# Kernel optimization log

Hardware: AMD Instinct MI355X
Metric: run time of the kernel (lower is better)

## Reference

```python
import jax, jax.numpy as jnp
import numpy as np

N = 100000          # nodes
E = 6400000         # edges (avg degree 64)
D = 512             # in_dim
NEG_SLOPE = 0.2     # PyG GATConv default leaky_relu slope


def setup_inputs() -> dict:
    key = jax.random.key(0)
    k1, k2, k3, k4, k5 = jax.random.split(key, 5)
    F = jax.random.normal(k1, (N, D), dtype=jnp.float32)
    edge_index = jax.random.randint(k2, (2, E), 0, N)
    W = jax.random.normal(k3, (D, 1), dtype=jnp.float32) * 0.05   # lin weight, out_channels=1
    att_src = jax.random.normal(k4, (1,), dtype=jnp.float32) * 0.1
    att_dst = jax.random.normal(k5, (1,), dtype=jnp.float32) * 0.1
    bias = jnp.zeros((1,), dtype=jnp.float32)
    return {"F": F, "edge_index": edge_index, "W": W,
            "att_src": att_src, "att_dst": att_dst, "bias": bias}


def reference(F, edge_index, W, att_src, att_dst, bias):
    n = F.shape[0]
    x = F @ W                                   # [N, 1] projected features
    # PyG GATConv default: add self-loops
    loops = jnp.arange(n, dtype=edge_index.dtype)
    src = jnp.concatenate([edge_index[0], loops])   # message source j
    dst = jnp.concatenate([edge_index[1], loops])   # message destination i
    a_src = (x * att_src).sum(-1)               # [N]
    a_dst = (x * att_dst).sum(-1)               # [N]
    logits = jax.nn.leaky_relu(a_src[src] + a_dst[dst], NEG_SLOPE)  # [E+N]
    # numerically stable per-destination softmax over incoming edges
    m = jax.ops.segment_max(logits, dst, num_segments=n)
    e = jnp.exp(logits - m[dst])
    denom = jax.ops.segment_sum(e, dst, num_segments=n)
    alpha = e / denom[dst]                      # [E+N]
    out = jax.ops.segment_sum(alpha[:, None] * x[src], dst, num_segments=n)  # [N,1]
    out = out + bias
    return out.squeeze()                        # [N]
```

## Files before the change

### kernel.cpp

```cpp
#include <hip/hip_runtime.h>

#define NEG_SLOPE 0.2f

#define DEN_SCALE 524288.0f
#define NUM_SCALE 32768.0f
#define INV_DEN_SCALE (1.0f / 524288.0f)
#define INV_NUM_SCALE (1.0f / 32768.0f)

#define RBITS 12
#define RSZ   4096
#define MAXNB 64
#define SSUB  16
#define EPT   8
#define P1BLK 256
#define CHUNK (P1BLK * EPT)

typedef float v4f __attribute__((ext_vector_type(4)));
typedef int   v4i __attribute__((ext_vector_type(4)));
typedef unsigned long long u64;
typedef unsigned int u32;

__global__ void gemv_rowdot(const float* __restrict__ F, const float* __restrict__ W,
                            float* __restrict__ x, int n, int d) {
    int wave = (blockIdx.x * blockDim.x + threadIdx.x) >> 6;
    int lane = threadIdx.x & 63;
    if (wave >= n) return;
    const v4f* f4 = (const v4f*)(F + (size_t)wave * d);
    const v4f* w4 = (const v4f*)W;
    int nv = d >> 2;
    float s = 0.f;
    #pragma unroll 2
    for (int k = lane; k < nv; k += 64) {
        v4f a = __builtin_nontemporal_load(&f4[k]);
        v4f b = w4[k];
        s += a.x * b.x + a.y * b.y + a.z * b.z + a.w * b.w;
    }
    #pragma unroll
    for (int off = 32; off; off >>= 1) s += __shfl_down(s, off, 64);
    if (lane == 0) x[wave] = s;
}

__device__ __forceinline__ u64 pack_edge(float e, float xs, int dlow) {
    int den = __float2int_rn(e * DEN_SCALE);
    den = min(den, (1 << 26) - 1);
    int num = __float2int_rn(e * xs * NUM_SCALE);
    num = max(min(num, (1 << 25) - 1), -((1 << 25) - 1));
    return (u64)(u32)dlow | ((u64)(u32)den << RBITS) | ((u64)((u32)num & 0x3FFFFFFu) << 38);
}

__global__ __launch_bounds__(P1BLK)
void bucket_scatter(const int* __restrict__ ei, const float* __restrict__ x,
                    const float* __restrict__ att_src_p, const float* __restrict__ att_dst_p,
                    u64* __restrict__ binbuf, u32* __restrict__ cnt,
                    u64* __restrict__ acc, int nedges, int nb, int capb) {
    __shared__ u32 lhist[MAXNB];
    __shared__ u32 lbase[MAXNB];
    const int tid = threadIdx.x;
    for (int b = tid; b < nb; b += P1BLK) lhist[b] = 0;
    __syncthreads();

    const long long base_e = (long long)blockIdx.x * CHUNK + (long long)tid * EPT;
    const float as = *att_src_p, ad = *att_dst_p;

    int se[EPT], de[EPT];
    if (((nedges & 3) == 0) && (base_e + EPT <= nedges)) {
        const v4i* sp = (const v4i*)(ei + base_e);
        const v4i* dp = (const v4i*)(ei + (size_t)nedges + base_e);
        v4i a0 = sp[0], a1 = sp[1], b0 = dp[0], b1 = dp[1];
        se[0] = a0.x; se[1] = a0.y; se[2] = a0.z; se[3] = a0.w;
        se[4] = a1.x; se[5] = a1.y; se[6] = a1.z; se[7] = a1.w;
        de[0] = b0.x; de[1] = b0.y; de[2] = b0.z; de[3] = b0.w;
        de[4] = b1.x; de[5] = b1.y; de[6] = b1.z; de[7] = b1.w;
    } else {
        #pragma unroll
        for (int t = 0; t < EPT; ++t) {
            long long idx = base_e + t;
            if (idx < nedges) { se[t] = ei[idx]; de[t] = ei[(size_t)nedges + idx]; }
            else { se[t] = -1; de[t] = -1; }
        }
    }

    float xs[EPT], xd[EPT];
    #pragma unroll
    for (int t = 0; t < EPT; ++t)
        if (se[t] >= 0) { xs[t] = x[se[t]]; xd[t] = x[de[t]]; }

    u64 pk[EPT]; u32 rk[EPT]; int bn[EPT];
    #pragma unroll
    for (int t = 0; t < EPT; ++t) {
        if (se[t] >= 0) {
            float v = xs[t] * as + xd[t] * ad;
            float logit = v > 0.f ? v : NEG_SLOPE * v;
            float e = __expf(logit);
            bn[t] = de[t] >> RBITS;
            pk[t] = pack_edge(e, xs[t], de[t] & (RSZ - 1));
            rk[t] = atomicAdd(&lhist[bn[t]], 1u);
        } else {
            bn[t] = -1;
        }
    }
    __syncthreads();
    if (tid < nb) lbase[tid] = atomicAdd(&cnt[tid], lhist[tid]);
    __syncthreads();
    #pragma unroll
    for (int t = 0; t < EPT; ++t) {
        if (bn[t] >= 0) {
            u32 slot = lbase[bn[t]] + rk[t];
            if (slot < (u32)capb) {
                binbuf[(size_t)bn[t] * (size_t)capb + slot] = pk[t];
            } else {
                int num = (int)((long long)pk[t] >> 38);
                u32 den = (u32)((pk[t] >> RBITS) & 0x3FFFFFFu);
                int dd = (bn[t] << RBITS) | (int)(pk[t] & (u64)(RSZ - 1));
                atomicAdd(&acc[dd], ((u64)(u32)num << 32) | (u64)den);
            }
        }
    }
}

__global__ __launch_bounds__(1024)
void bin_reduce(const u64* __restrict__ binbuf, const u32* __restrict__ cnt,
                u64* __restrict__ partial, int nb, int capb) {
    __shared__ u64 lacc[RSZ];
    const int b = blockIdx.x / SSUB;
    const int s = blockIdx.x % SSUB;
    const int tid = threadIdx.x;
    #pragma unroll
    for (int r = tid; r < RSZ; r += 1024) lacc[r] = 0ull;
    __syncthreads();

    u32 cb = cnt[b];
    if (cb > (u32)capb) cb = (u32)capb;
    u32 lo = (u32)(((u64)cb * (u32)s) / SSUB);
    u32 hi = (u32)(((u64)cb * (u32)(s + 1)) / SSUB);
    const u64* src = binbuf + (size_t)b * (size_t)capb;
    for (u32 k = lo + tid; k < hi; k += 1024) {
        u64 p = src[k];
        u32 r   = (u32)(p & (u64)(RSZ - 1));
        u32 den = (u32)((p >> RBITS) & 0x3FFFFFFu);
        int num = (int)((long long)p >> 38);
        atomicAdd(&lacc[r], ((u64)(u32)num << 32) | (u64)den);
    }
    __syncthreads();
    u64* dstp = partial + (size_t)blockIdx.x * RSZ;
    #pragma unroll
    for (int r = tid; r < RSZ; r += 1024) dstp[r] = lacc[r];
}

__global__ void finalize2(const u64* __restrict__ partial, const u64* __restrict__ acc,
                          const float* __restrict__ x,
                          const float* __restrict__ att_src_p,
                          const float* __restrict__ att_dst_p,
                          const float* __restrict__ bias, float* __restrict__ out, int n) {
    int i = blockIdx.x * blockDim.x + threadIdx.x;
    if (i >= n) return;
    int b = i >> RBITS, r = i & (RSZ - 1);
    u64 t = acc[i];
    const u64* pp = partial + ((size_t)b * SSUB) * RSZ + r;
    #pragma unroll
    for (int s = 0; s < SSUB; ++s) t += pp[(size_t)s * RSZ];
    float xi = x[i];
    float v = xi * (*att_src_p + *att_dst_p);
    float logit = v > 0.f ? v : NEG_SLOPE * v;
    float es = __expf(logit);
    float num = (float)(int)(t >> 32) * INV_NUM_SCALE;
    float den = (float)(u32)(t & 0xFFFFFFFFull) * INV_DEN_SCALE;
    out[i] = (num + es * xi) / (den + es) + *bias;
}

__device__ __forceinline__ void edge_one(float xs, float xd, float as, float ad,
                                         int d, u64* __restrict__ acc) {
    float v = xs * as + xd * ad;
    float logit = v > 0.f ? v : NEG_SLOPE * v;
    float e = __expf(logit);
    u32 den_fx = (u32)__float2int_rn(e * DEN_SCALE);
    int num_fx = __float2int_rn(e * xs * NUM_SCALE);
    atomicAdd(&acc[d], ((u64)(u32)num_fx << 32) | (u64)den_fx);
}

__global__ void edge_accum4(const int* __restrict__ ei, const float* __restrict__ x,
                            const float* __restrict__ att_src_p,
                            const float* __restrict__ att_dst_p,
                            u64* __restrict__ acc, int nedges) {
    int nq = nedges >> 2;
    int i = blockIdx.x * blockDim.x + threadIdx.x;
    if (i >= nq) return;
    const v4i* s4 = (const v4i*)ei;
    const v4i* d4 = (const v4i*)(ei + nedges);
    v4i s = s4[i], d = d4[i];
    float as = *att_src_p, ad = *att_dst_p;
    float xs0 = x[s.x], xs1 = x[s.y], xs2 = x[s.z], xs3 = x[s.w];
    float xd0 = x[d.x], xd1 = x[d.y], xd2 = x[d.z], xd3 = x[d.w];
    edge_one(xs0, xd0, as, ad, d.x, acc);
    edge_one(xs1, xd1, as, ad, d.y, acc);
    edge_one(xs2, xd2, as, ad, d.z, acc);
    edge_one(xs3, xd3, as, ad, d.w, acc);
}

__global__ void edge_accum1(const int* __restrict__ ei, const float* __restrict__ x,
                            const float* __restrict__ att_src_p,
                            const float* __restrict__ att_dst_p,
                            u64* __restrict__ acc, int nedges) {
    int i = blockIdx.x * blockDim.x + threadIdx.x;
    if (i >= nedges) return;
    int s = ei[i], d = ei[nedges + i];
    edge_one(x[s], x[d], *att_src_p, *att_dst_p, d, acc);
}

__global__ void finalize_atomic(const u64* __restrict__ acc, const float* __restrict__ x,
                                const float* __restrict__ att_src_p,
                                const float* __restrict__ att_dst_p,
                                const float* __restrict__ bias, float* __restrict__ out,
                                int n) {
    int i = blockIdx.x * blockDim.x + threadIdx.x;
    if (i >= n) return;
    float xi = x[i];
    float v = xi * (*att_src_p + *att_dst_p);
    float logit = v > 0.f ? v : NEG_SLOPE * v;
    float es = __expf(logit);
    u64 a = acc[i];
    float num = (float)(int)(a >> 32) * INV_NUM_SCALE;
    float den = (float)(u32)(a & 0xFFFFFFFFull) * INV_DEN_SCALE;
    out[i] = (num + es * xi) / (den + es) + *bias;
}

extern "C" void kernel_launch(void* const* d_in, const int* in_sizes, int n_in,
                              void* d_out, int out_size, void* d_ws, size_t ws_size,
                              hipStream_t stream) {
    const float* F       = (const float*)d_in[0];
    const int*   ei      = (const int*)d_in[1];
    const float* W       = (const float*)d_in[2];
    const float* att_src = (const float*)d_in[3];
    const float* att_dst = (const float*)d_in[4];
    const float* bias    = (const float*)d_in[5];
    float* out = (float*)d_out;

    int d = in_sizes[2];
    int n = in_sizes[0] / d;
    int e = in_sizes[1] / 2;

    int nb = (n + RSZ - 1) >> RBITS;
    size_t capb_s = ((size_t)e * RSZ) / (size_t)n;
    capb_s += capb_s / 16 + 4096;
    int capb = (int)capb_s;

    size_t off_x   = 0;
    size_t off_acc = ((size_t)n * 4 + 7) & ~(size_t)7;
    size_t off_cnt = off_acc + (size_t)n * 8;
    size_t off_par = (off_cnt + (size_t)nb * 4 + 7) & ~(size_t)7;
    size_t off_bin = off_par + (size_t)nb * SSUB * RSZ * 8;
    size_t needed  = off_bin + (size_t)nb * capb_s * 8;

    float* x  = (float*)((char*)d_ws + off_x);
    u64* acc  = (u64*)((char*)d_ws + off_acc);
    u32* cnt  = (u32*)((char*)d_ws + off_cnt);
    u64* par  = (u64*)((char*)d_ws + off_par);
    u64* bin  = (u64*)((char*)d_ws + off_bin);

    bool fast = (nb <= MAXNB) && (needed <= ws_size) && (e > 0) && (n > 0);

    gemv_rowdot<<<(n + 3) / 4, 256, 0, stream>>>(F, W, x, n, d);

    if (fast) {
        (void)hipMemsetAsync(acc, 0, (size_t)n * 8 + (size_t)nb * 4, stream);
        int nblk1 = (int)(((long long)e + CHUNK - 1) / CHUNK);
        bucket_scatter<<<nblk1, P1BLK, 0, stream>>>(ei, x, att_src, att_dst,
                                                    bin, cnt, acc, e, nb, capb);
        bin_reduce<<<nb * SSUB, 1024, 0, stream>>>(bin, cnt, par, nb, capb);
        finalize2<<<(n + 255) / 256, 256, 0, stream>>>(par, acc, x, att_src, att_dst,
                                                       bias, out, n);
    } else {
        (void)hipMemsetAsync(acc, 0, (size_t)n * 8, stream);
        if (e > 0) {
            if ((e & 3) == 0) {
                edge_accum4<<<((e >> 2) + 255) / 256, 256, 0, stream>>>(
                    ei, x, att_src, att_dst, acc, e);
            } else {
                edge_accum1<<<(e + 255) / 256, 256, 0, stream>>>(
                    ei, x, att_src, att_dst, acc, e);
            }
        }
        finalize_atomic<<<(n + 255) / 256, 256, 0, stream>>>(acc, x, att_src, att_dst,
                                                             bias, out, n);
    }
}
```

Measured before the change: 377.5 us.

## Fuse GEMV with edge bucketing and defer logit computation to bin reduce

The bucket scatter no longer depends on x. It packs (src, dst-low) into 32-bit bin entries, and its blocks run in the same launch as the GEMV blocks, so the edge-index bucketing overlaps with the large F read. Logit, exp and fixed-point packing move to bin_reduce, which keeps the bucket's destination x values in shared memory and gathers x[src] from global. Bin entries are half as wide, overflow edges go to a separate buffer handled by a new kernel, and EPT/SSUB are raised. The cost is an extra launch and random x[src] gathers in the reduce phase.

```diff
diff --git a/kernel.cpp b/kernel.cpp
--- a/kernel.cpp
+++ b/kernel.cpp
@@ -10,15 +10,26 @@
 #define RBITS 12
 #define RSZ   4096
 #define MAXNB 64
-#define SSUB  16
-#define EPT   8
+#define SSUB  20
+#define EPT   16
 #define P1BLK 256
 #define CHUNK (P1BLK * EPT)
+#define P2BLK 1024
 
 typedef float v4f __attribute__((ext_vector_type(4)));
 typedef int   v4i __attribute__((ext_vector_type(4)));
 typedef unsigned long long u64;
 typedef unsigned int u32;
+
+__device__ __forceinline__ void edge_one(float xs, float xd, float as, float ad,
+                                         int d, u64* __restrict__ acc) {
+    float v = xs * as + xd * ad;
+    float logit = v > 0.f ? v : NEG_SLOPE * v;
+    float e = __expf(logit);
+    u32 den_fx = (u32)__float2int_rn(e * DEN_SCALE);
+    int num_fx = __float2int_rn(e * xs * NUM_SCALE);
+    atomicAdd(&acc[d], ((u64)(u32)num_fx << 32) | (u64)den_fx);
+}
 
 __global__ void gemv_rowdot(const float* __restrict__ F, const float* __restrict__ W,
                             float* __restrict__ x, int n, int d) {
@@ -40,19 +51,32 @@
     if (lane == 0) x[wave] = s;
 }
 
-__device__ __forceinline__ u64 pack_edge(float e, float xs, int dlow) {
-    int den = __float2int_rn(e * DEN_SCALE);
-    den = min(den, (1 << 26) - 1);
-    int num = __float2int_rn(e * xs * NUM_SCALE);
-    num = max(min(num, (1 << 25) - 1), -((1 << 25) - 1));
-    return (u64)(u32)dlow | ((u64)(u32)den << RBITS) | ((u64)((u32)num & 0x3FFFFFFu) << 38);
-}
-
 __global__ __launch_bounds__(P1BLK)
-void bucket_scatter(const int* __restrict__ ei, const float* __restrict__ x,
-                    const float* __restrict__ att_src_p, const float* __restrict__ att_dst_p,
-                    u64* __restrict__ binbuf, u32* __restrict__ cnt,
-                    u64* __restrict__ acc, int nedges, int nb, int capb) {
+void gemv_and_scatter(const float* __restrict__ F, const float* __restrict__ W,
+                      float* __restrict__ x, int n, int d,
+                      const int* __restrict__ ei, u32* __restrict__ binbuf,
+                      u32* __restrict__ cnt, u64* __restrict__ ovf,
+                      int nedges, int nb, int capb, int nsblk, u32 ovfcap) {
+    if ((int)blockIdx.x >= nsblk) {
+        int gblk = (int)blockIdx.x - nsblk;
+        int wave = gblk * 4 + ((int)threadIdx.x >> 6);
+        int lane = threadIdx.x & 63;
+        if (wave >= n) return;
+        const v4f* f4 = (const v4f*)(F + (size_t)wave * d);
+        const v4f* w4 = (const v4f*)W;
+        int nv = d >> 2;
+        float s = 0.f;
+        #pragma unroll 2
+        for (int k = lane; k < nv; k += 64) {
+            v4f a = __builtin_nontemporal_load(&f4[k]);
+            v4f b = w4[k];
+            s += a.x * b.x + a.y * b.y + a.z * b.z + a.w * b.w;
+        }
+        #pragma unroll
+        for (int off = 32; off; off >>= 1) s += __shfl_down(s, off, 64);
+        if (lane == 0) x[wave] = s;
+        return;
+    }
     __shared__ u32 lhist[MAXNB];
     __shared__ u32 lbase[MAXNB];
     const int tid = threadIdx.x;
@@ -60,17 +84,20 @@
     __syncthreads();
 
     const long long base_e = (long long)blockIdx.x * CHUNK + (long long)tid * EPT;
-    const float as = *att_src_p, ad = *att_dst_p;
 
     int se[EPT], de[EPT];
     if (((nedges & 3) == 0) && (base_e + EPT <= nedges)) {
         const v4i* sp = (const v4i*)(ei + base_e);
         const v4i* dp = (const v4i*)(ei + (size_t)nedges + base_e);
-        v4i a0 = sp[0], a1 = sp[1], b0 = dp[0], b1 = dp[1];
-        se[0] = a0.x; se[1] = a0.y; se[2] = a0.z; se[3] = a0.w;
-        se[4] = a1.x; se[5] = a1.y; se[6] = a1.z; se[7] = a1.w;
-        de[0] = b0.x; de[1] = b0.y; de[2] = b0.z; de[3] = b0.w;
-        de[4] = b1.x; de[5] = b1.y; de[6] = b1.z; de[7] = b1.w;
+        #pragma unroll
+        for (int q = 0; q < EPT / 4; ++q) {
+            v4i a = __builtin_nontemporal_load(&sp[q]);
+            v4i b = __builtin_nontemporal_load(&dp[q]);
+            se[4 * q + 0] = a.x; se[4 * q + 1] = a.y;
+            se[4 * q + 2] = a.z; se[4 * q + 3] = a.w;
+            de[4 * q + 0] = b.x; de[4 * q + 1] = b.y;
+            de[4 * q + 2] = b.z; de[4 * q + 3] = b.w;
+        }
     } else {
         #pragma unroll
         for (int t = 0; t < EPT; ++t) {
@@ -80,20 +107,12 @@
         }
     }
 
-    float xs[EPT], xd[EPT];
-    #pragma unroll
-    for (int t = 0; t < EPT; ++t)
-        if (se[t] >= 0) { xs[t] = x[se[t]]; xd[t] = x[de[t]]; }
-
-    u64 pk[EPT]; u32 rk[EPT]; int bn[EPT];
+    u32 pk[EPT], rk[EPT]; int bn[EPT];
     #pragma unroll
     for (int t = 0; t < EPT; ++t) {
         if (se[t] >= 0) {
-            float v = xs[t] * as + xd[t] * ad;
-            float logit = v > 0.f ? v : NEG_SLOPE * v;
-            float e = __expf(logit);
             bn[t] = de[t] >> RBITS;
-            pk[t] = pack_edge(e, xs[t], de[t] & (RSZ - 1));
+            pk[t] = ((u32)se[t] << RBITS) | (u32)(de[t] & (RSZ - 1));
             rk[t] = atomicAdd(&lhist[bn[t]], 1u);
         } else {
             bn[t] = -1;
@@ -109,42 +128,72 @@
             if (slot < (u32)capb) {
                 binbuf[(size_t)bn[t] * (size_t)capb + slot] = pk[t];
             } else {
-                int num = (int)((long long)pk[t] >> 38);
-                u32 den = (u32)((pk[t] >> RBITS) & 0x3FFFFFFu);
-                int dd = (bn[t] << RBITS) | (int)(pk[t] & (u64)(RSZ - 1));
-                atomicAdd(&acc[dd], ((u64)(u32)num << 32) | (u64)den);
+                u32 os = atomicAdd(&cnt[MAXNB], 1u);
+                if (os < ovfcap)
+                    ovf[os] = ((u64)(u32)se[t] << 32) | (u64)(u32)de[t];
             }
         }
     }
 }
 
-__global__ __launch_bounds__(1024)
-void bin_reduce(const u64* __restrict__ binbuf, const u32* __restrict__ cnt,
-                u64* __restrict__ partial, int nb, int capb) {
+__global__ void overflow_fix(const u64* __restrict__ ovf, const u32* __restrict__ cnt,
+                             const float* __restrict__ x,
+                             const float* __restrict__ att_src_p,
+                             const float* __restrict__ att_dst_p,
+                             u64* __restrict__ acc, u32 ovfcap) {
+    u32 m = cnt[MAXNB];
+    if (m > ovfcap) m = ovfcap;
+    float as = *att_src_p, ad = *att_dst_p;
+    for (u32 i = blockIdx.x * blockDim.x + threadIdx.x; i < m;
+         i += gridDim.x * blockDim.x) {
+        u64 p = ovf[i];
+        int s = (int)(p >> 32), dd = (int)(p & 0xFFFFFFFFull);
+        edge_one(x[s], x[dd], as, ad, dd, acc);
+    }
+}
+
+__global__ __launch_bounds__(P2BLK)
+void bin_reduce(const u32* __restrict__ binbuf, const u32* __restrict__ cnt,
+                const float* __restrict__ x,
+                const float* __restrict__ att_src_p, const float* __restrict__ att_dst_p,
+                u64* __restrict__ partial, int n, int capb) {
     __shared__ u64 lacc[RSZ];
+    __shared__ float lx[RSZ];
     const int b = blockIdx.x / SSUB;
     const int s = blockIdx.x % SSUB;
     const int tid = threadIdx.x;
-    #pragma unroll
-    for (int r = tid; r < RSZ; r += 1024) lacc[r] = 0ull;
-    __syncthreads();
-
+    const int base = b << RBITS;
+    #pragma unroll
+    for (int r = tid; r < RSZ; r += P2BLK) {
+        lacc[r] = 0ull;
+        int idx = base + r;
+        lx[r] = (idx < n) ? x[idx] : 0.f;
+    }
+    __syncthreads();
+
+    const float as = *att_src_p, ad = *att_dst_p;
     u32 cb = cnt[b];
     if (cb > (u32)capb) cb = (u32)capb;
     u32 lo = (u32)(((u64)cb * (u32)s) / SSUB);
     u32 hi = (u32)(((u64)cb * (u32)(s + 1)) / SSUB);
-    const u64* src = binbuf + (size_t)b * (size_t)capb;
-    for (u32 k = lo + tid; k < hi; k += 1024) {
-        u64 p = src[k];
-        u32 r   = (u32)(p & (u64)(RSZ - 1));
-        u32 den = (u32)((p >> RBITS) & 0x3FFFFFFu);
-        int num = (int)((long long)p >> 38);
-        atomicAdd(&lacc[r], ((u64)(u32)num << 32) | (u64)den);
+    const u32* src = binbuf + (size_t)b * (size_t)capb;
+    for (u32 k = lo + tid; k < hi; k += P2BLK) {
+        u32 p = src[k];
+        int sj   = (int)(p >> RBITS);
+        int dlow = (int)(p & (RSZ - 1));
+        float xs = x[sj];
+        float xd = lx[dlow];
+        float v = xs * as + xd * ad;
+        float logit = v > 0.f ? v : NEG_SLOPE * v;
+        float e = __expf(logit);
+        u32 den = (u32)__float2int_rn(e * DEN_SCALE);
+        int num = __float2int_rn(e * xs * NUM_SCALE);
+        atomicAdd(&lacc[dlow], ((u64)(u32)num << 32) | (u64)den);
     }
     __syncthreads();
     u64* dstp = partial + (size_t)blockIdx.x * RSZ;
     #pragma unroll
-    for (int r = tid; r < RSZ; r += 1024) dstp[r] = lacc[r];
+    for (int r = tid; r < RSZ; r += P2BLK) dstp[r] = lacc[r];
 }
 
 __global__ void finalize2(const u64* __restrict__ partial, const u64* __restrict__ acc,
@@ -166,16 +215,6 @@
     float num = (float)(int)(t >> 32) * INV_NUM_SCALE;
     float den = (float)(u32)(t & 0xFFFFFFFFull) * INV_DEN_SCALE;
     out[i] = (num + es * xi) / (den + es) + *bias;
-}
-
-__device__ __forceinline__ void edge_one(float xs, float xd, float as, float ad,
-                                         int d, u64* __restrict__ acc) {
-    float v = xs * as + xd * ad;
-    float logit = v > 0.f ? v : NEG_SLOPE * v;
-    float e = __expf(logit);
-    u32 den_fx = (u32)__float2int_rn(e * DEN_SCALE);
-    int num_fx = __float2int_rn(e * xs * NUM_SCALE);
-    atomicAdd(&acc[d], ((u64)(u32)num_fx << 32) | (u64)den_fx);
 }
 
 __global__ void edge_accum4(const int* __restrict__ ei, const float* __restrict__ x,
@@ -240,37 +279,43 @@
     int e = in_sizes[1] / 2;
 
     int nb = (n + RSZ - 1) >> RBITS;
-    size_t capb_s = ((size_t)e * RSZ) / (size_t)n;
+    size_t capb_s = ((size_t)e * RSZ) / (size_t)(n > 0 ? n : 1);
     capb_s += capb_s / 16 + 4096;
     int capb = (int)capb_s;
+    u32 ovfcap = (u32)e;
 
     size_t off_x   = 0;
     size_t off_acc = ((size_t)n * 4 + 7) & ~(size_t)7;
     size_t off_cnt = off_acc + (size_t)n * 8;
-    size_t off_par = (off_cnt + (size_t)nb * 4 + 7) & ~(size_t)7;
-    size_t off_bin = off_par + (size_t)nb * SSUB * RSZ * 8;
-    size_t needed  = off_bin + (size_t)nb * capb_s * 8;
+    size_t off_par = (off_cnt + (size_t)(MAXNB + 1) * 4 + 7) & ~(size_t)7;
+    size_t off_ovf = off_par + (size_t)nb * SSUB * RSZ * 8;
+    size_t off_bin = off_ovf + (size_t)ovfcap * 8;
+    size_t needed  = off_bin + (size_t)nb * capb_s * 4;
 
     float* x  = (float*)((char*)d_ws + off_x);
     u64* acc  = (u64*)((char*)d_ws + off_acc);
     u32* cnt  = (u32*)((char*)d_ws + off_cnt);
     u64* par  = (u64*)((char*)d_ws + off_par);
-    u64* bin  = (u64*)((char*)d_ws + off_bin);
-
-    bool fast = (nb <= MAXNB) && (needed <= ws_size) && (e > 0) && (n > 0);
-
-    gemv_rowdot<<<(n + 3) / 4, 256, 0, stream>>>(F, W, x, n, d);
+    u64* ovf  = (u64*)((char*)d_ws + off_ovf);
+    u32* bin  = (u32*)((char*)d_ws + off_bin);
+
+    bool fast = (nb <= MAXNB) && (n <= (1 << (32 - RBITS))) &&
+                (needed <= ws_size) && (e > 0) && (n > 0);
 
     if (fast) {
-        (void)hipMemsetAsync(acc, 0, (size_t)n * 8 + (size_t)nb * 4, stream);
-        int nblk1 = (int)(((long long)e + CHUNK - 1) / CHUNK);
-        bucket_scatter<<<nblk1, P1BLK, 0, stream>>>(ei, x, att_src, att_dst,
-                                                    bin, cnt, acc, e, nb, capb);
-        bin_reduce<<<nb * SSUB, 1024, 0, stream>>>(bin, cnt, par, nb, capb);
+        (void)hipMemsetAsync(acc, 0, (size_t)n * 8 + (size_t)(MAXNB + 1) * 4, stream);
+        int nsblk = (int)(((long long)e + CHUNK - 1) / CHUNK);
+        int ngblk = (n + 3) / 4;
+        gemv_and_scatter<<<nsblk + ngblk, P1BLK, 0, stream>>>(
+            F, W, x, n, d, ei, bin, cnt, ovf, e, nb, capb, nsblk, ovfcap);
+        overflow_fix<<<256, 256, 0, stream>>>(ovf, cnt, x, att_src, att_dst, acc, ovfcap);
+        bin_reduce<<<nb * SSUB, P2BLK, 0, stream>>>(bin, cnt, x, att_src, att_dst,
+                                                    par, n, capb);
         finalize2<<<(n + 255) / 256, 256, 0, stream>>>(par, acc, x, att_src, att_dst,
                                                        bias, out, n);
     } else {
         (void)hipMemsetAsync(acc, 0, (size_t)n * 8, stream);
+        gemv_rowdot<<<(n + 3) / 4, 256, 0, stream>>>(F, W, x, n, d);
         if (e > 0) {
             if ((e & 3) == 0) {
                 edge_accum4<<<((e >> 2) + 255) / 256, 256, 0, stream>>>(
```

Measured after the change: 362.9 us. 1.04x faster.
